# Kernel optimization log

Hardware: AMD Instinct MI355X
Metric: run time of the kernel (lower is better)

Reference implementation:

```python
import jax, jax.numpy as jnp
import numpy as np

H, D = 16, 64          # num_attention_heads, attention_head_size
SPAN = 512             # att_span == max_relative_positions (q==k==2048 > 512)


def _split_heads(x):
    # [B, S, H*D] -> [B, H, S, D]
    B, S, _ = x.shape
    return x.reshape(B, S, H, D).transpose(0, 2, 1, 3)


def setup_inputs() -> dict:
    key = jax.random.key(0)
    ks = jax.random.split(key, 8)
    B, S, hid = 2, 2048, 1024
    sc = 1.0 / np.sqrt(hid).astype(np.float32)  # keep activations O(1)
    return {
        "hidden_states": jax.random.normal(ks[0], (B, S, hid), jnp.float32),
        "rel_embeddings": jax.random.normal(ks[1], (2 * SPAN, hid), jnp.float32),
        "Wq": jax.random.normal(ks[2], (hid, hid), jnp.float32) * sc,
        "bq": jnp.zeros((hid,), jnp.float32),
        "Wk": jax.random.normal(ks[3], (hid, hid), jnp.float32) * sc,
        "bk": jnp.zeros((hid,), jnp.float32),
        "Wv": jax.random.normal(ks[4], (hid, hid), jnp.float32) * sc,
        "bv": jnp.zeros((hid,), jnp.float32),
        "Wpk": jax.random.normal(ks[5], (hid, hid), jnp.float32) * sc,
        "Wpq": jax.random.normal(ks[6], (hid, hid), jnp.float32) * sc,
        "bpq": jnp.zeros((hid,), jnp.float32),
    }


def reference(hidden_states, rel_embeddings, Wq, bq, Wk, bk, Wv, bv, Wpk, Wpq, bpq):
    B, S, hid = hidden_states.shape
    q = _split_heads(hidden_states @ Wq + bq)   # [B,H,S,D]
    k = _split_heads(hidden_states @ Wk + bk)
    v = _split_heads(hidden_states @ Wv + bv)

    scale_factor = 3  # 1 + c2p + p2c
    scores = jnp.einsum('bhqd,bhkd->bhqk', q, k)

    # relative positions (query_size == key_size == S)
    ids = jnp.arange(S)
    rel_pos = ids[:, None] - ids[None, :]                      # [S,S]

    # positional projections: [2*SPAN, hid] -> [H, 2*SPAN, D]
    pos_k = (rel_embeddings @ Wpk).reshape(2 * SPAN, H, D).transpose(1, 0, 2)
    pos_q = (rel_embeddings @ Wpq + bpq).reshape(2 * SPAN, H, D).transpose(1, 0, 2)

    # content->position
    c2p_att = jnp.einsum('bhqd,hrd->bhqr', q, pos_k)           # [B,H,S,2*SPAN]
    c2p_pos = jnp.clip(rel_pos + SPAN, 0, 2 * SPAN - 1)        # [S,S]
    c2p = jnp.take_along_axis(c2p_att, c2p_pos[None, None], axis=-1)

    # position->content (pos_query scaled by sqrt(D*scale_factor) as in DeBERTa)
    pos_q = pos_q / jnp.sqrt(jnp.asarray(D * scale_factor, hidden_states.dtype))
    p2c_att = jnp.einsum('bhkd,hrd->bhkr', k, pos_q)           # [B,H,S,2*SPAN]
    p2c_pos = jnp.clip(-rel_pos + SPAN, 0, 2 * SPAN - 1)
    p2c = jnp.take_along_axis(p2c_att, p2c_pos[None, None], axis=-1).swapaxes(-1, -2)

    scores = (scores + c2p + p2c) / np.sqrt(D).astype(np.float32)
    probs = jax.nn.softmax(scores, axis=-1)
    ctx = jnp.einsum('bhqk,bhkd->bhqd', probs, v)
    return ctx.transpose(0, 2, 1, 3).reshape(B, S, hid)
```

## Files before the change

### kernel.cpp

```cpp
#include <hip/hip_runtime.h>
#include <math.h>

#define HID 1024
#define NH 16
#define DH 64
#define SEQ 2048
#define NB 2
#define SPAN 512
#define PSTR 72
#define VSTR 66
#define BST  132

typedef __attribute__((ext_vector_type(8))) _Float16 f16x8;
typedef __attribute__((ext_vector_type(4))) _Float16 f16x4;
typedef __attribute__((ext_vector_type(4))) float f32x4;

__device__ __forceinline__ float dpp_max16(float x) {
  int v;
  v = __builtin_amdgcn_update_dpp(0, __builtin_bit_cast(int, x), 0x128, 0xF, 0xF, true);
  x = fmaxf(x, __builtin_bit_cast(float, v));
  v = __builtin_amdgcn_update_dpp(0, __builtin_bit_cast(int, x), 0x124, 0xF, 0xF, true);
  x = fmaxf(x, __builtin_bit_cast(float, v));
  v = __builtin_amdgcn_update_dpp(0, __builtin_bit_cast(int, x), 0x122, 0xF, 0xF, true);
  x = fmaxf(x, __builtin_bit_cast(float, v));
  v = __builtin_amdgcn_update_dpp(0, __builtin_bit_cast(int, x), 0x121, 0xF, 0xF, true);
  return fmaxf(x, __builtin_bit_cast(float, v));
}
__device__ __forceinline__ float dpp_sum16(float x) {
  int v;
  v = __builtin_amdgcn_update_dpp(0, __builtin_bit_cast(int, x), 0x128, 0xF, 0xF, true);
  x += __builtin_bit_cast(float, v);
  v = __builtin_amdgcn_update_dpp(0, __builtin_bit_cast(int, x), 0x124, 0xF, 0xF, true);
  x += __builtin_bit_cast(float, v);
  v = __builtin_amdgcn_update_dpp(0, __builtin_bit_cast(int, x), 0x122, 0xF, 0xF, true);
  x += __builtin_bit_cast(float, v);
  v = __builtin_amdgcn_update_dpp(0, __builtin_bit_cast(int, x), 0x121, 0xF, 0xF, true);
  return x + __builtin_bit_cast(float, v);
}

__global__ __launch_bounds__(256)
void cvt16(const float* __restrict__ src, _Float16* __restrict__ dst, int n4) {
  int i = blockIdx.x * 256 + threadIdx.x;
  const int stride = gridDim.x * 256;
  for (; i < n4; i += stride) {
    float4 v = ((const float4*)src)[i];
    f16x4 o;
    o.x = (_Float16)v.x; o.y = (_Float16)v.y;
    o.z = (_Float16)v.z; o.w = (_Float16)v.w;
    ((f16x4*)dst)[i] = o;
  }
}

__global__ __launch_bounds__(256)
void transW(const float* __restrict__ W0, const float* __restrict__ W1,
            const float* __restrict__ W2, const float* __restrict__ W3,
            const float* __restrict__ W4, _Float16* __restrict__ Wt) {
  const int z = blockIdx.z;
  const float* W = z == 0 ? W0 : z == 1 ? W1 : z == 2 ? W2 : z == 3 ? W3 : W4;
  _Float16* out = Wt + (size_t)z * HID * HID;
  const int k0 = blockIdx.x * 64, n0 = blockIdx.y * 64;
  __shared__ _Float16 t[64][72];
  const int tid = threadIdx.x;
  #pragma unroll
  for (int p = 0; p < 4; ++p) {
    int idx = tid + p * 256;
    int row = idx >> 4, c4 = idx & 15;
    float4 v = *(const float4*)&W[(size_t)(k0 + row) * HID + n0 + c4 * 4];
    t[c4 * 4 + 0][row] = (_Float16)v.x;
    t[c4 * 4 + 1][row] = (_Float16)v.y;
    t[c4 * 4 + 2][row] = (_Float16)v.z;
    t[c4 * 4 + 3][row] = (_Float16)v.w;
  }
  __syncthreads();
  #pragma unroll
  for (int p = 0; p < 2; ++p) {
    int idx = tid + p * 256;
    int row = idx >> 3, c8 = idx & 7;
    *(f16x8*)&out[(size_t)(n0 + row) * HID + k0 + c8 * 8] = *(const f16x8*)&t[row][c8 * 8];
  }
}

__global__ __launch_bounds__(256)
void gemm_all(const _Float16* __restrict__ A16, const _Float16* __restrict__ R16,
              const _Float16* __restrict__ Wt,
              const float* __restrict__ bq, const float* __restrict__ bk,
              const float* __restrict__ bv, const float* __restrict__ bpq,
              _Float16* __restrict__ qo, _Float16* __restrict__ ko,
              _Float16* __restrict__ vo, _Float16* __restrict__ pko,
              _Float16* __restrict__ pqo, float qscale, float pqscale) {
  const int z = blockIdx.z;
  if (z >= 3 && blockIdx.y >= 8) return;
  const _Float16* A = (z < 3) ? A16 : R16;
  const _Float16* B = Wt + (size_t)z * HID * HID;
  const float* bias = z == 0 ? bq : z == 1 ? bk : z == 2 ? bv : z == 3 ? (const float*)nullptr : bpq;
  _Float16* C = z == 0 ? qo : z == 1 ? ko : z == 2 ? vo : z == 3 ? pko : pqo;
  const float scale = z == 0 ? qscale : z == 4 ? pqscale : 1.0f;

  __shared__ _Float16 As[128 * 40];
  __shared__ _Float16 Bs[128 * 40];
  const int tid = threadIdx.x;
  const int m0 = blockIdx.y * 128, n0 = blockIdx.x * 128;
  const int w = tid >> 6, l = tid & 63;
  const int wr = w >> 1, wc = w & 1;
  const int lr = l & 15, lh = l >> 4;

  f32x4 acc[4][4];
  #pragma unroll
  for (int m = 0; m < 4; ++m)
    #pragma unroll
    for (int n = 0; n < 4; ++n)
      acc[m][n] = (f32x4){0.f, 0.f, 0.f, 0.f};

  for (int k0 = 0; k0 < HID; k0 += 32) {
    __syncthreads();
    #pragma unroll
    for (int p = 0; p < 2; ++p) {
      int idx = tid + p * 256;
      int row = idx >> 2, c = idx & 3;
      *(f16x8*)&As[row * 40 + c * 8] = *(const f16x8*)&A[(size_t)(m0 + row) * HID + k0 + c * 8];
      *(f16x8*)&Bs[row * 40 + c * 8] = *(const f16x8*)&B[(size_t)(n0 + row) * HID + k0 + c * 8];
    }
    __syncthreads();

    f16x8 af[4], bfr[4];
    #pragma unroll
    for (int m = 0; m < 4; ++m)
      af[m] = *(const f16x8*)&As[(wr * 64 + m * 16 + lr) * 40 + lh * 8];
    #pragma unroll
    for (int n = 0; n < 4; ++n)
      bfr[n] = *(const f16x8*)&Bs[(wc * 64 + n * 16 + lr) * 40 + lh * 8];
    #pragma unroll
    for (int m = 0; m < 4; ++m)
      #pragma unroll
      for (int n = 0; n < 4; ++n)
        acc[m][n] = __builtin_amdgcn_mfma_f32_16x16x32_f16(af[m], bfr[n], acc[m][n], 0, 0, 0);
  }

  #pragma unroll
  for (int n = 0; n < 4; ++n) {
    int col = n0 + wc * 64 + n * 16 + lr;
    float bv_ = bias ? bias[col] : 0.0f;
    #pragma unroll
    for (int m = 0; m < 4; ++m)
      #pragma unroll
      for (int r = 0; r < 4; ++r) {
        int row = m0 + wr * 64 + m * 16 + lh * 4 + r;
        C[(size_t)row * HID + col] = (_Float16)((acc[m][n][r] + bv_) * scale);
      }
  }
}

__global__ __launch_bounds__(256, 2)
void attn_mfma(const _Float16* __restrict__ qg, const _Float16* __restrict__ kg,
               const _Float16* __restrict__ vg, const _Float16* __restrict__ pkg,
               const _Float16* __restrict__ pqg, float* __restrict__ outg) {
  const int q0 = blockIdx.x * 64;
  const int h = blockIdx.y, b = blockIdx.z;
  const int tid = threadIdx.x;
  const int w = tid >> 6, l = tid & 63;
  const int lr = l & 15, lh = l >> 4;
  const size_t hoff = (size_t)h * DH;

  __shared__ _Float16 ks[64 * PSTR];
  __shared__ _Float16 vst[64 * VSTR];
  __shared__ _Float16 ps[64 * PSTR];
  __shared__ _Float16 posA[128 * PSTR];
  __shared__ _Float16 posB[128 * PSTR];
  _Float16* c2pb = posA;
  _Float16* p2cb = posB;

  f16x8 aq[2];
  #pragma unroll
  for (int kk = 0; kk < 2; ++kk)
    aq[kk] = *(const f16x8*)&qg[((size_t)(b * SEQ + q0 + w * 16 + lr)) * HID + hoff + kk * 32 + lh * 8];

  f32x4 accO[4];
  float m_[4], l_[4];
  #pragma unroll
  for (int r = 0; r < 4; ++r) { m_[r] = -1e30f; l_[r] = 0.0f; }
  #pragma unroll
  for (int nt = 0; nt < 4; ++nt) accO[nt] = (f32x4){0.f, 0.f, 0.f, 0.f};

  const int vd4 = tid & 15, vkq = tid >> 4;

  for (int k0 = 0; k0 < SEQ; k0 += 64) {
    __syncthreads();
    for (int idx = tid; idx < 64 * 8; idx += 256) {
      int row = idx >> 3, c = idx & 7;
      *(f16x8*)&ks[row * PSTR + c * 8] =
          *(const f16x8*)&kg[((size_t)(b * SEQ + k0 + row)) * HID + hoff + c * 8];
    }
    {
      f16x4 vr[4];
      #pragma unroll
      for (int j = 0; j < 4; ++j)
        vr[j] = *(const f16x4*)&vg[((size_t)(b * SEQ + k0 + vkq * 4 + j)) * HID + hoff + vd4 * 4];
      #pragma unroll
      for (int di = 0; di < 4; ++di) {
        f16x4 wv;
        wv.x = vr[0][di]; wv.y = vr[1][di]; wv.z = vr[2][di]; wv.w = vr[3][di];
        *(f16x4*)&vst[(vd4 * 4 + di) * VSTR + vkq * 4] = wv;
      }
    }
    const int r_lo = min(max(q0 - k0 - 63 + SPAN, 0), 2 * SPAN - 1);
    const int r_hi = min(max(q0 - k0 + 63 + SPAN, 0), 2 * SPAN - 1);
    const int nr = r_hi - r_lo + 1;
    const int bt_lim = (nr + 15) >> 4;
    for (int idx = tid; idx < nr * 8; idx += 256) {
      int row = idx >> 3, c = idx & 7;
      size_t gb = ((size_t)(r_lo + row)) * HID + hoff + c * 8;
      *(f16x8*)&posA[row * PSTR + c * 8] = *(const f16x8*)&pkg[gb];
      *(f16x8*)&posB[row * PSTR + c * 8] = *(const f16x8*)&pqg[gb];
    }
    __syncthreads();

    f16x8 ak[2];
    #pragma unroll
    for (int kk = 0; kk < 2; ++kk)
      ak[kk] = *(const f16x8*)&ks[(w * 16 + lr) * PSTR + kk * 32 + lh * 8];

    f32x4 sqk[4];
    #pragma unroll
    for (int nt = 0; nt < 4; ++nt) sqk[nt] = (f32x4){0.f, 0.f, 0.f, 0.f};
    #pragma unroll
    for (int nt = 0; nt < 4; ++nt)
      #pragma unroll
      for (int kk = 0; kk < 2; ++kk) {
        f16x8 bk = *(const f16x8*)&ks[(nt * 16 + lr) * PSTR + kk * 32 + lh * 8];
        sqk[nt] = __builtin_amdgcn_mfma_f32_16x16x32_f16(aq[kk], bk, sqk[nt], 0, 0, 0);
      }

    f32x4 bandA[8], bandB[8];
    #pragma unroll
    for (int bt = 0; bt < 8; ++bt) {
      bandA[bt] = (f32x4){0.f, 0.f, 0.f, 0.f};
      bandB[bt] = (f32x4){0.f, 0.f, 0.f, 0.f};
    }
    #pragma unroll
    for (int bt = 0; bt < 8; ++bt)
      if (bt < bt_lim)
        #pragma unroll
        for (int kk = 0; kk < 2; ++kk) {
          f16x8 bp = *(const f16x8*)&posA[(bt * 16 + lr) * PSTR + kk * 32 + lh * 8];
          bandA[bt] = __builtin_amdgcn_mfma_f32_16x16x32_f16(aq[kk], bp, bandA[bt], 0, 0, 0);
        }
    #pragma unroll
    for (int bt = 0; bt < 8; ++bt)
      if (bt < bt_lim)
        #pragma unroll
        for (int kk = 0; kk < 2; ++kk) {
          f16x8 bp = *(const f16x8*)&posB[(bt * 16 + lr) * PSTR + kk * 32 + lh * 8];
          bandB[bt] = __builtin_amdgcn_mfma_f32_16x16x32_f16(ak[kk], bp, bandB[bt], 0, 0, 0);
        }
    __syncthreads();

    #pragma unroll
    for (int bt = 0; bt < 8; ++bt)
      if (bt < bt_lim) {
        #pragma unroll
        for (int r = 0; r < 4; ++r) {
          int rowi = w * 16 + lh * 4 + r;
          c2pb[rowi * BST + bt * 16 + lr] = (_Float16)bandA[bt][r];
          p2cb[rowi * BST + bt * 16 + lr] = (_Float16)bandB[bt][r];
        }
      }
    __syncthreads();

    const int rfix = (q0 - k0 + SPAN) - r_lo;
    float pc1[4];
    if (nr == 1) {
      #pragma unroll
      for (int nt = 0; nt < 4; ++nt) pc1[nt] = (float)p2cb[(nt * 16 + lr) * BST];
    }
    #pragma unroll
    for (int r = 0; r < 4; ++r) {
      int qi = w * 16 + lh * 4 + r;
      float sc[4];
      if (nr == 1) {
        float cA = (float)c2pb[qi * BST];
        #pragma unroll
        for (int nt = 0; nt < 4; ++nt)
          sc[nt] = sqk[nt][r] + cA + pc1[nt];
      } else {
        #pragma unroll
        for (int nt = 0; nt < 4; ++nt) {
          int ki = nt * 16 + lr;
          int ri = min(max(rfix + qi - ki, 0), nr - 1);
          sc[nt] = sqk[nt][r] + (float)c2pb[qi * BST + ri] + (float)p2cb[ki * BST + ri];
        }
      }
      float mx = dpp_max16(fmaxf(fmaxf(sc[0], sc[1]), fmaxf(sc[2], sc[3])));
      float mnew = fmaxf(m_[r], mx);
      float alpha = __expf(m_[r] - mnew);
      float s0 = 0.0f;
      #pragma unroll
      for (int nt = 0; nt < 4; ++nt) {
        float p = __expf(sc[nt] - mnew);
        s0 += p;
        ps[qi * PSTR + (nt ^ lh) * 16 + lr] = (_Float16)p;
      }
      l_[r] = l_[r] * alpha + s0;
      m_[r] = mnew;
      #pragma unroll
      for (int nt = 0; nt < 4; ++nt) accO[nt][r] *= alpha;
    }

    f16x8 pa[2];
    const int keyr = lr >> 2;
    #pragma unroll
    for (int kk = 0; kk < 2; ++kk) {
      int blk = (kk * 2 + (lh >> 1)) ^ keyr;
      pa[kk] = *(const f16x8*)&ps[(w * 16 + lr) * PSTR + blk * 16 + (lh & 1) * 8];
    }
    #pragma unroll
    for (int nt = 0; nt < 4; ++nt)
      #pragma unroll
      for (int kk = 0; kk < 2; ++kk) {
        f16x8 vb = *(const f16x8*)&vst[(nt * 16 + lr) * VSTR + kk * 32 + lh * 8];
        accO[nt] = __builtin_amdgcn_mfma_f32_16x16x32_f16(pa[kk], vb, accO[nt], 0, 0, 0);
      }
  }

  #pragma unroll
  for (int r = 0; r < 4; ++r) {
    float inv = 1.0f / dpp_sum16(l_[r]);
    int row = q0 + w * 16 + lh * 4 + r;
    #pragma unroll
    for (int nt = 0; nt < 4; ++nt) {
      int col = h * DH + nt * 16 + lr;
      outg[((size_t)(b * SEQ + row)) * HID + col] = accO[nt][r] * inv;
    }
  }
}

extern "C" void kernel_launch(void* const* d_in, const int* in_sizes, int n_in,
                              void* d_out, int out_size, void* d_ws, size_t ws_size,
                              hipStream_t stream) {
  const float* hs  = (const float*)d_in[0];
  const float* rel = (const float*)d_in[1];
  const float* Wq  = (const float*)d_in[2];
  const float* bq  = (const float*)d_in[3];
  const float* Wk  = (const float*)d_in[4];
  const float* bk  = (const float*)d_in[5];
  const float* Wv  = (const float*)d_in[6];
  const float* bv  = (const float*)d_in[7];
  const float* Wpk = (const float*)d_in[8];
  const float* Wpq = (const float*)d_in[9];
  const float* bpq = (const float*)d_in[10];
  float* out = (float*)d_out;

  _Float16* ws = (_Float16*)d_ws;
  _Float16* q   = ws;
  _Float16* k   = ws + 4194304;
  _Float16* v   = ws + 8388608;
  _Float16* pk  = ws + 12582912;
  _Float16* pq  = ws + 13631488;
  _Float16* A16 = ws + 14680064;
  _Float16* R16 = ws + 18874368;
  _Float16* Wt  = ws + 19922944;

  const float qscale  = 0.125f;
  const float pqscale = 1.0f / (8.0f * sqrtf(192.0f));

  dim3 blk(256);
  cvt16<<<dim3(2048), blk, 0, stream>>>(hs, A16, (NB * SEQ * HID) / 4);
  cvt16<<<dim3(1024), blk, 0, stream>>>(rel, R16, (2 * SPAN * HID) / 4);
  transW<<<dim3(16, 16, 5), blk, 0, stream>>>(Wq, Wk, Wv, Wpk, Wpq, Wt);

  gemm_all<<<dim3(HID / 128, (NB * SEQ) / 128, 5), blk, 0, stream>>>(
      A16, R16, Wt, bq, bk, bv, bpq, q, k, v, pk, pq, qscale, pqscale);

  dim3 ga(SEQ / 64, NH, NB);
  attn_mfma<<<ga, blk, 0, stream>>>(q, k, v, pk, pq, out);
}
```

Measured before the change: 367.7 us.

## Read positional embeddings directly from global, shrink LDS, raise occupancy to 3

Drops the LDS staging of the pos_k/pos_q band tiles. The band MFMAs now load their B operands straight from global memory, and the A and B band MFMAs are interleaved. The P tile reuses the c2p buffer with a new swizzle, one __syncthreads is removed, and launch bounds rise to 3 blocks per CU because LDS use is smaller. The aim is higher occupancy and fewer barriers, at the cost of uncached, uncoalesced global loads in the inner loop and more register pressure.

```diff
diff --git a/kernel.cpp b/kernel.cpp
--- a/kernel.cpp
+++ b/kernel.cpp
@@ -8,7 +8,7 @@
 #define NB 2
 #define SPAN 512
 #define PSTR 72
-#define VSTR 66
+#define VSTR 72
 #define BST  132
 
 typedef __attribute__((ext_vector_type(8))) _Float16 f16x8;
@@ -150,7 +150,7 @@
   }
 }
 
-__global__ __launch_bounds__(256, 2)
+__global__ __launch_bounds__(256, 3)
 void attn_mfma(const _Float16* __restrict__ qg, const _Float16* __restrict__ kg,
                const _Float16* __restrict__ vg, const _Float16* __restrict__ pkg,
                const _Float16* __restrict__ pqg, float* __restrict__ outg) {
@@ -163,11 +163,8 @@
 
   __shared__ _Float16 ks[64 * PSTR];
   __shared__ _Float16 vst[64 * VSTR];
-  __shared__ _Float16 ps[64 * PSTR];
-  __shared__ _Float16 posA[128 * PSTR];
-  __shared__ _Float16 posB[128 * PSTR];
-  _Float16* c2pb = posA;
-  _Float16* p2cb = posB;
+  __shared__ _Float16 c2pb[64 * BST];
+  __shared__ _Float16 p2cb[64 * BST];
 
   f16x8 aq[2];
   #pragma unroll
@@ -206,12 +203,6 @@
     const int r_hi = min(max(q0 - k0 + 63 + SPAN, 0), 2 * SPAN - 1);
     const int nr = r_hi - r_lo + 1;
     const int bt_lim = (nr + 15) >> 4;
-    for (int idx = tid; idx < nr * 8; idx += 256) {
-      int row = idx >> 3, c = idx & 7;
-      size_t gb = ((size_t)(r_lo + row)) * HID + hoff + c * 8;
-      *(f16x8*)&posA[row * PSTR + c * 8] = *(const f16x8*)&pkg[gb];
-      *(f16x8*)&posB[row * PSTR + c * 8] = *(const f16x8*)&pqg[gb];
-    }
     __syncthreads();
 
     f16x8 ak[2];
@@ -238,21 +229,16 @@
     }
     #pragma unroll
     for (int bt = 0; bt < 8; ++bt)
-      if (bt < bt_lim)
+      if (bt < bt_lim) {
+        size_t prow = ((size_t)(r_lo + bt * 16 + lr)) * HID + hoff + lh * 8;
         #pragma unroll
         for (int kk = 0; kk < 2; ++kk) {
-          f16x8 bp = *(const f16x8*)&posA[(bt * 16 + lr) * PSTR + kk * 32 + lh * 8];
-          bandA[bt] = __builtin_amdgcn_mfma_f32_16x16x32_f16(aq[kk], bp, bandA[bt], 0, 0, 0);
+          f16x8 bpA = *(const f16x8*)&pkg[prow + kk * 32];
+          f16x8 bpB = *(const f16x8*)&pqg[prow + kk * 32];
+          bandA[bt] = __builtin_amdgcn_mfma_f32_16x16x32_f16(aq[kk], bpA, bandA[bt], 0, 0, 0);
+          bandB[bt] = __builtin_amdgcn_mfma_f32_16x16x32_f16(ak[kk], bpB, bandB[bt], 0, 0, 0);
         }
-    #pragma unroll
-    for (int bt = 0; bt < 8; ++bt)
-      if (bt < bt_lim)
-        #pragma unroll
-        for (int kk = 0; kk < 2; ++kk) {
-          f16x8 bp = *(const f16x8*)&posB[(bt * 16 + lr) * PSTR + kk * 32 + lh * 8];
-          bandB[bt] = __builtin_amdgcn_mfma_f32_16x16x32_f16(ak[kk], bp, bandB[bt], 0, 0, 0);
-        }
-    __syncthreads();
+      }
 
     #pragma unroll
     for (int bt = 0; bt < 8; ++bt)
@@ -297,7 +283,7 @@
       for (int nt = 0; nt < 4; ++nt) {
         float p = __expf(sc[nt] - mnew);
         s0 += p;
-        ps[qi * PSTR + (nt ^ lh) * 16 + lr] = (_Float16)p;
+        c2pb[qi * BST + ((nt + 2 * lh) & 3) * 16 + lr] = (_Float16)p;
       }
       l_[r] = l_[r] * alpha + s0;
       m_[r] = mnew;
@@ -306,11 +292,14 @@
     }
 
     f16x8 pa[2];
-    const int keyr = lr >> 2;
     #pragma unroll
     for (int kk = 0; kk < 2; ++kk) {
-      int blk = (kk * 2 + (lh >> 1)) ^ keyr;
-      pa[kk] = *(const f16x8*)&ps[(w * 16 + lr) * PSTR + blk * 16 + (lh & 1) * 8];
+      int blk = (2 * kk + (lh >> 1) + 2 * (lr >> 2)) & 3;
+      const _Float16* base = &c2pb[(w * 16 + lr) * BST + blk * 16 + (lh & 1) * 8];
+      f16x4 lo = *(const f16x4*)base;
+      f16x4 hi = *(const f16x4*)(base + 4);
+      #pragma unroll
+      for (int e = 0; e < 4; ++e) { pa[kk][e] = lo[e]; pa[kk][4 + e] = hi[e]; }
     }
     #pragma unroll
     for (int nt = 0; nt < 4; ++nt)
```

Measured after the change: 570.4 us. 1.55x slower.

## Prefetch next K/V/pos tiles into registers and transpose band scratch layout

Applied to the files above, without the earlier changes.

Global loads of the next key, value and positional tiles are issued into registers right after the current tile is written to shared memory, so global latency overlaps the MFMA and softmax work of the current iteration. The band results are now stored transposed (position-major, PSTR stride) with vectorised f16x4 writes instead of scalar stores. s_setprio hints are added around the MFMA sections. The register prefetch raises VGPR pressure, which could hurt occupancy under the 256x2 launch bounds.

```diff
diff --git a/kernel.cpp b/kernel.cpp
--- a/kernel.cpp
+++ b/kernel.cpp
@@ -9,7 +9,6 @@
 #define SPAN 512
 #define PSTR 72
 #define VSTR 66
-#define BST  132
 
 typedef __attribute__((ext_vector_type(8))) _Float16 f16x8;
 typedef __attribute__((ext_vector_type(4))) _Float16 f16x4;
@@ -166,8 +165,8 @@
   __shared__ _Float16 ps[64 * PSTR];
   __shared__ _Float16 posA[128 * PSTR];
   __shared__ _Float16 posB[128 * PSTR];
-  _Float16* c2pb = posA;
-  _Float16* p2cb = posB;
+  _Float16* c2pT = posA;
+  _Float16* p2cT = posB;
 
   f16x8 aq[2];
   #pragma unroll
@@ -183,37 +182,86 @@
 
   const int vd4 = tid & 15, vkq = tid >> 4;
 
+  f16x8 kreg[2], pAreg[4], pBreg[4];
+  f16x4 vreg[4];
+  {
+    #pragma unroll
+    for (int p = 0; p < 2; ++p) {
+      int idx = tid + p * 256, row = idx >> 3, c = idx & 7;
+      kreg[p] = *(const f16x8*)&kg[((size_t)(b * SEQ + row)) * HID + hoff + c * 8];
+    }
+    #pragma unroll
+    for (int j = 0; j < 4; ++j)
+      vreg[j] = *(const f16x4*)&vg[((size_t)(b * SEQ + vkq * 4 + j)) * HID + hoff + vd4 * 4];
+    int r_lo1 = min(max(q0 - 63 + SPAN, 0), 2 * SPAN - 1);
+    int r_hi1 = min(max(q0 + 63 + SPAN, 0), 2 * SPAN - 1);
+    int nr1 = r_hi1 - r_lo1 + 1;
+    #pragma unroll
+    for (int p = 0; p < 4; ++p) {
+      int idx = tid + p * 256;
+      if (idx < nr1 * 8) {
+        int row = idx >> 3, c = idx & 7;
+        size_t gb = ((size_t)(r_lo1 + row)) * HID + hoff + c * 8;
+        pAreg[p] = *(const f16x8*)&pkg[gb];
+        pBreg[p] = *(const f16x8*)&pqg[gb];
+      }
+    }
+  }
+
   for (int k0 = 0; k0 < SEQ; k0 += 64) {
-    __syncthreads();
-    for (int idx = tid; idx < 64 * 8; idx += 256) {
-      int row = idx >> 3, c = idx & 7;
-      *(f16x8*)&ks[row * PSTR + c * 8] =
-          *(const f16x8*)&kg[((size_t)(b * SEQ + k0 + row)) * HID + hoff + c * 8];
-    }
-    {
-      f16x4 vr[4];
-      #pragma unroll
-      for (int j = 0; j < 4; ++j)
-        vr[j] = *(const f16x4*)&vg[((size_t)(b * SEQ + k0 + vkq * 4 + j)) * HID + hoff + vd4 * 4];
-      #pragma unroll
-      for (int di = 0; di < 4; ++di) {
-        f16x4 wv;
-        wv.x = vr[0][di]; wv.y = vr[1][di]; wv.z = vr[2][di]; wv.w = vr[3][di];
-        *(f16x4*)&vst[(vd4 * 4 + di) * VSTR + vkq * 4] = wv;
-      }
-    }
     const int r_lo = min(max(q0 - k0 - 63 + SPAN, 0), 2 * SPAN - 1);
     const int r_hi = min(max(q0 - k0 + 63 + SPAN, 0), 2 * SPAN - 1);
     const int nr = r_hi - r_lo + 1;
     const int bt_lim = (nr + 15) >> 4;
-    for (int idx = tid; idx < nr * 8; idx += 256) {
-      int row = idx >> 3, c = idx & 7;
-      size_t gb = ((size_t)(r_lo + row)) * HID + hoff + c * 8;
-      *(f16x8*)&posA[row * PSTR + c * 8] = *(const f16x8*)&pkg[gb];
-      *(f16x8*)&posB[row * PSTR + c * 8] = *(const f16x8*)&pqg[gb];
-    }
-    __syncthreads();
-
+
+    __syncthreads();
+    #pragma unroll
+    for (int p = 0; p < 2; ++p) {
+      int idx = tid + p * 256, row = idx >> 3, c = idx & 7;
+      *(f16x8*)&ks[row * PSTR + c * 8] = kreg[p];
+    }
+    #pragma unroll
+    for (int di = 0; di < 4; ++di) {
+      f16x4 wv;
+      wv.x = vreg[0][di]; wv.y = vreg[1][di]; wv.z = vreg[2][di]; wv.w = vreg[3][di];
+      *(f16x4*)&vst[(vd4 * 4 + di) * VSTR + vkq * 4] = wv;
+    }
+    #pragma unroll
+    for (int p = 0; p < 4; ++p) {
+      int idx = tid + p * 256;
+      if (idx < nr * 8) {
+        int row = idx >> 3, c = idx & 7;
+        *(f16x8*)&posA[row * PSTR + c * 8] = pAreg[p];
+        *(f16x8*)&posB[row * PSTR + c * 8] = pBreg[p];
+      }
+    }
+    const int k1 = k0 + 64;
+    if (k1 < SEQ) {
+      #pragma unroll
+      for (int p = 0; p < 2; ++p) {
+        int idx = tid + p * 256, row = idx >> 3, c = idx & 7;
+        kreg[p] = *(const f16x8*)&kg[((size_t)(b * SEQ + k1 + row)) * HID + hoff + c * 8];
+      }
+      #pragma unroll
+      for (int j = 0; j < 4; ++j)
+        vreg[j] = *(const f16x4*)&vg[((size_t)(b * SEQ + k1 + vkq * 4 + j)) * HID + hoff + vd4 * 4];
+      int r_lo1 = min(max(q0 - k1 - 63 + SPAN, 0), 2 * SPAN - 1);
+      int r_hi1 = min(max(q0 - k1 + 63 + SPAN, 0), 2 * SPAN - 1);
+      int nr1 = r_hi1 - r_lo1 + 1;
+      #pragma unroll
+      for (int p = 0; p < 4; ++p) {
+        int idx = tid + p * 256;
+        if (idx < nr1 * 8) {
+          int row = idx >> 3, c = idx & 7;
+          size_t gb = ((size_t)(r_lo1 + row)) * HID + hoff + c * 8;
+          pAreg[p] = *(const f16x8*)&pkg[gb];
+          pBreg[p] = *(const f16x8*)&pqg[gb];
+        }
+      }
+    }
+    __syncthreads();
+
+    __builtin_amdgcn_s_setprio(1);
     f16x8 ak[2];
     #pragma unroll
     for (int kk = 0; kk < 2; ++kk)
@@ -252,17 +300,20 @@
           f16x8 bp = *(const f16x8*)&posB[(bt * 16 + lr) * PSTR + kk * 32 + lh * 8];
           bandB[bt] = __builtin_amdgcn_mfma_f32_16x16x32_f16(ak[kk], bp, bandB[bt], 0, 0, 0);
         }
+    __builtin_amdgcn_s_setprio(0);
     __syncthreads();
 
     #pragma unroll
     for (int bt = 0; bt < 8; ++bt)
       if (bt < bt_lim) {
+        f16x4 wa, wb;
         #pragma unroll
         for (int r = 0; r < 4; ++r) {
-          int rowi = w * 16 + lh * 4 + r;
-          c2pb[rowi * BST + bt * 16 + lr] = (_Float16)bandA[bt][r];
-          p2cb[rowi * BST + bt * 16 + lr] = (_Float16)bandB[bt][r];
+          wa[r] = (_Float16)bandA[bt][r];
+          wb[r] = (_Float16)bandB[bt][r];
         }
+        *(f16x4*)&c2pT[(bt * 16 + lr) * PSTR + w * 16 + lh * 4] = wa;
+        *(f16x4*)&p2cT[(bt * 16 + lr) * PSTR + w * 16 + lh * 4] = wb;
       }
     __syncthreads();
 
@@ -270,14 +321,14 @@
     float pc1[4];
     if (nr == 1) {
       #pragma unroll
-      for (int nt = 0; nt < 4; ++nt) pc1[nt] = (float)p2cb[(nt * 16 + lr) * BST];
+      for (int nt = 0; nt < 4; ++nt) pc1[nt] = (float)p2cT[nt * 16 + lr];
     }
     #pragma unroll
     for (int r = 0; r < 4; ++r) {
       int qi = w * 16 + lh * 4 + r;
       float sc[4];
       if (nr == 1) {
-        float cA = (float)c2pb[qi * BST];
+        float cA = (float)c2pT[qi];
         #pragma unroll
         for (int nt = 0; nt < 4; ++nt)
           sc[nt] = sqk[nt][r] + cA + pc1[nt];
@@ -286,7 +337,7 @@
         for (int nt = 0; nt < 4; ++nt) {
           int ki = nt * 16 + lr;
           int ri = min(max(rfix + qi - ki, 0), nr - 1);
-          sc[nt] = sqk[nt][r] + (float)c2pb[qi * BST + ri] + (float)p2cb[ki * BST + ri];
+          sc[nt] = sqk[nt][r] + (float)c2pT[ri * PSTR + qi] + (float)p2cT[ri * PSTR + ki];
         }
       }
       float mx = dpp_max16(fmaxf(fmaxf(sc[0], sc[1]), fmaxf(sc[2], sc[3])));
@@ -297,7 +348,7 @@
       for (int nt = 0; nt < 4; ++nt) {
         float p = __expf(sc[nt] - mnew);
         s0 += p;
-        ps[qi * PSTR + (nt ^ lh) * 16 + lr] = (_Float16)p;
+        ps[qi * PSTR + ((nt ^ lh) * 16) + lr] = (_Float16)p;
       }
       l_[r] = l_[r] * alpha + s0;
       m_[r] = mnew;
@@ -305,6 +356,7 @@
       for (int nt = 0; nt < 4; ++nt) accO[nt][r] *= alpha;
     }
 
+    __builtin_amdgcn_s_setprio(1);
     f16x8 pa[2];
     const int keyr = lr >> 2;
     #pragma unroll
@@ -319,6 +371,7 @@
         f16x8 vb = *(const f16x8*)&vst[(nt * 16 + lr) * VSTR + kk * 32 + lh * 8];
         accO[nt] = __builtin_amdgcn_mfma_f32_16x16x32_f16(pa[kk], vb, accO[nt], 0, 0, 0);
       }
+    __builtin_amdgcn_s_setprio(0);
   }
 
   #pragma unroll
```

New measurement: 308.7 us. 16.0% less time.
